# Kernel optimization log

Measured on AMD Instinct MI355X. Metric: run time of the kernel, lower is better.

Reference implementation:

```python
import jax, jax.numpy as jnp
import numpy as np
from functools import partial

EPS = 1e-12  # F.normalize eps (clamp_min on the norm)


def conv2d(x, w, b, groups=1):
    # x: [B, Cin, H, W], w: [Cout, Cin//groups, 3, 3], 'same' padding, stride 1
    y = jax.lax.conv_general_dilated(
        x, w, window_strides=(1, 1), padding='SAME',
        dimension_numbers=('NCHW', 'OIHW', 'NCHW'),
        feature_group_count=groups)
    return y + b[None, :, None, None]


def setup_inputs() -> dict:
    key = jax.random.key(0)
    ks = jax.random.split(key, 8)
    B, C, H, W = 16, 256, 32, 32
    HW = H * W
    T = 2  # tasks: seg, depth
    return {
        'features_seg': jax.random.normal(ks[0], (B, C, H, W), jnp.float32),
        'features_depth': jax.random.normal(ks[1], (B, C, H, W), jnp.float32),
        'proj_w_seg': jax.random.normal(ks[2], (C, C, 3, 3), jnp.float32) * 0.02,
        'proj_b_seg': jnp.zeros((C,), jnp.float32),
        'proj_w_depth': jax.random.normal(ks[3], (C, C, 3, 3), jnp.float32) * 0.02,
        'proj_b_depth': jnp.zeros((C,), jnp.float32),
        'fusion_w': jax.random.normal(ks[4], (HW, T, 3, 3), jnp.float32) * 0.02,
        'fusion_b': jnp.zeros((HW,), jnp.float32),
    }


def reference(features_seg, features_depth, proj_w_seg, proj_b_seg,
              proj_w_depth, proj_b_depth, fusion_w, fusion_b):
    gamma = 0.5
    feats = [features_seg, features_depth]
    proj = [(proj_w_seg, proj_b_seg), (proj_w_depth, proj_b_depth)]
    B, C, H, W = features_seg.shape
    HW = H * W

    # Per-task cosine-similarity affinity matrices [B, HW, HW]
    Ms = []
    for f in feats:
        fv = f.reshape(B, C, HW)
        fn = fv / jnp.maximum(jnp.linalg.norm(fv, axis=1, keepdims=True), EPS)
        aff = jnp.einsum('bci,bcj->bij', fn, fn)  # [B, HW, HW]
        Ms.append(aff.reshape(B, HW, H, W))

    # Stack on dim=2 then flatten -> interleaved channels [B, HW*T, H, W]
    M = jnp.stack(Ms, axis=2).reshape(B, -1, H, W)
    M = conv2d(M, fusion_w, fusion_b, groups=HW)  # [B, HW, H, W]

    attention = M.reshape(B, HW, HW).transpose(0, 2, 1)  # [B, HW, HW]

    outs = []
    for f, (w, b) in zip(feats, proj):
        value = conv2d(f, w, b).reshape(B, C, HW)          # [B, C, HW]
        attended = jnp.einsum('bck,bkj->bcj', value, attention)
        attended = attended.reshape(B, C, H, W)
        outs.append(gamma * attended + (1.0 - gamma) * f)
    return tuple(outs)
```

## Files before the change

### kernel.cpp

```cpp
#include <hip/hip_runtime.h>
#include <hip/hip_bf16.h>

typedef __bf16 bf16;
typedef __attribute__((ext_vector_type(8))) __bf16 bf16x8;
typedef __attribute__((ext_vector_type(4))) __bf16 bf16x4v;
typedef __attribute__((ext_vector_type(4))) float f32x4;

#define B_  16
#define C_  256
#define HW_ 1024

__device__ __forceinline__ void gll16(const bf16* g, bf16* l) {
  __builtin_amdgcn_global_load_lds((const __attribute__((address_space(1))) void*)g,
                                   (__attribute__((address_space(3))) void*)l, 16, 0, 0);
}

__global__ void prep_kernel(const float* __restrict__ f0, const float* __restrict__ f1,
                            bf16* __restrict__ fT, float* __restrict__ rn) {
  __shared__ float sm[256][33];
  __shared__ float ps[8][32];
  int z = blockIdx.y, t = z >> 4, b = z & 15;
  int k0 = blockIdx.x * 32;
  int tid = threadIdx.x;
  const float* fb = (t ? f1 : f0) + (size_t)b * C_ * HW_ + k0;
  int kk = tid & 31, cg = tid >> 5;
  float ssq = 0.f;
  #pragma unroll
  for (int i = 0; i < 32; ++i) {
    int c = cg + i * 8;
    float v = fb[(size_t)c * HW_ + kk];
    sm[c][kk] = v;
    ssq += v * v;
  }
  ps[cg][kk] = ssq;
  __syncthreads();
  if (tid < 32) {
    float s = 0.f;
    #pragma unroll
    for (int r = 0; r < 8; ++r) s += ps[r][tid];
    rn[z * 1024 + k0 + tid] = 1.f / fmaxf(sqrtf(s), 1e-12f);
  }
  int kl = tid >> 3, c0 = (tid & 7) * 32;
  bf16* dst = fT + ((size_t)z * HW_ + k0 + kl) * C_ + c0;
  #pragma unroll
  for (int u = 0; u < 4; ++u) {
    bf16x8 vv;
    #pragma unroll
    for (int e = 0; e < 8; ++e) vv[e] = (bf16)sm[c0 + u * 8 + e][kl];
    *(bf16x8*)(dst + u * 8) = vv;
  }
}

__global__ void fusion_conv2(const bf16* __restrict__ aff, const float* __restrict__ fw,
                             const float* __restrict__ fb, bf16* __restrict__ M) {
  __shared__ float sa[2][1024];
  int bi = blockIdx.x;
  int i = bi & 1023, b = bi >> 10;
  int tid = threadIdx.x;
  #pragma unroll
  for (int t = 0; t < 2; ++t) {
    const bf16* arow = aff + (((size_t)t * 16 + b) * 1024 + i) * 1024;
    bf16x4v ch = ((const bf16x4v*)arow)[tid];
    sa[t][tid * 4 + 0] = (float)ch[0];
    sa[t][tid * 4 + 1] = (float)ch[1];
    sa[t][tid * 4 + 2] = (float)ch[2];
    sa[t][tid * 4 + 3] = (float)ch[3];
  }
  float wgt[2][9];
  #pragma unroll
  for (int t = 0; t < 2; ++t)
    #pragma unroll
    for (int q = 0; q < 9; ++q) wgt[t][q] = fw[i * 18 + t * 9 + q];
  float bias = fb[i];
  __syncthreads();
  #pragma unroll
  for (int s0 = 0; s0 < 4; ++s0) {
    int s = tid + s0 * 256;
    int h = s >> 5, w = s & 31;
    float acc = bias;
    #pragma unroll
    for (int kh = 0; kh < 3; ++kh) {
      int hh = h + kh - 1;
      if ((unsigned)hh < 32u) {
        #pragma unroll
        for (int kw = 0; kw < 3; ++kw) {
          int ww = w + kw - 1;
          if ((unsigned)ww < 32u) {
            acc += wgt[0][kh * 3 + kw] * sa[0][hh * 32 + ww];
            acc += wgt[1][kh * 3 + kw] * sa[1][hh * 32 + ww];
          }
        }
      }
    }
    M[((size_t)bi << 10) + s] = (bf16)acc;
  }
}

__global__ void reorder_w(const float* __restrict__ w0, const float* __restrict__ w1,
                          bf16* __restrict__ y) {
  int i = blockIdx.x * 256 + threadIdx.x;
  int t = i / 589824, r2 = i % 589824;
  int c = r2 / 2304, r = r2 % 2304;
  int cin = r / 9, d = r % 9;
  y[(size_t)t * 589824 + c * 2304 + d * 256 + cin] = (bf16)(t ? w1 : w0)[r2];
}

template<int MODE, int TN>
__global__ __launch_bounds__(256)
void gemm_nt(const bf16* __restrict__ A, long long sA,
             const bf16* __restrict__ Bm, long long sB, int K,
             bf16* __restrict__ Cb, long long sC,
             const float* __restrict__ x0, const float* __restrict__ x1,
             float* __restrict__ Co) {
  constexpr int FJ   = (TN == 128) ? 4 : 2;
  __shared__ bf16 As[128 * 64];
  __shared__ bf16 Bs[TN * ((MODE == 3) ? 72 : 64)];
  const int z = blockIdx.z, t = z >> 4;
  const bf16* Ab = A + (size_t)(MODE == 3 ? t : z) * sA;
  const bf16* Bb = Bm + (size_t)(MODE == 2 ? (z & 15) : z) * sB;
  const int m0 = blockIdx.y * 128, n0 = blockIdx.x * TN;
  const int tid = threadIdx.x;
  const int lane = tid & 63, wave = tid >> 6;
  const int wm = (wave >> 1) * 64, wn = (wave & 1) * (TN / 2);
  const int fr = lane & 15, fq = lane >> 4;

  f32x4 acc[4][FJ];
  #pragma unroll
  for (int i = 0; i < 4; ++i)
    #pragma unroll
    for (int j = 0; j < FJ; ++j) acc[i][j] = 0.f;

  for (int k0 = 0; k0 < K; k0 += 64) {
    #pragma unroll
    for (int s = 0; s < 4; ++s) {
      int q = (wave * 4 + s) * 64 + lane;
      int row = q >> 3, c = (q & 7) ^ (row & 7);
      int lb = __builtin_amdgcn_readfirstlane((wave * 4 + s) * 512);
      gll16(Ab + (size_t)(m0 + row) * K + k0 + c * 8, As + lb);
    }
    if (MODE == 3) {
      int d = k0 >> 8;
      int kh = d / 3 - 1, kw = d % 3 - 1;
      int cin0 = k0 & 255;
      #pragma unroll
      for (int s = 0; s < TN / 32; ++s) {
        int q = tid + s * 256;
        int row = q >> 3, col = (q & 7) * 8;
        int j = n0 + row;
        int h = (j >> 5) + kh, w = (j & 31) + kw;
        float4 v = make_float4(0.f, 0.f, 0.f, 0.f);
        if ((unsigned)h < 32u && (unsigned)w < 32u)
          v = *(const float4*)(Bb + (size_t)(h * 32 + w) * C_ + cin0 + col);
        *(float4*)(&Bs[row * 72 + col]) = v;
      }
    } else {
      #pragma unroll
      for (int s = 0; s < TN / 32; ++s) {
        int q = (wave * (TN / 32) + s) * 64 + lane;
        int row = q >> 3, c = (q & 7) ^ (row & 7);
        int lb = __builtin_amdgcn_readfirstlane((wave * (TN / 32) + s) * 512);
        gll16(Bb + (size_t)(n0 + row) * K + k0 + c * 8, Bs + lb);
      }
    }
    __syncthreads();
    #pragma unroll
    for (int kk = 0; kk < 64; kk += 32) {
      bf16x8 af[4], bfr[FJ];
      #pragma unroll
      for (int i = 0; i < 4; ++i) {
        int rr = wm + i * 16 + fr;
        int p = ((kk >> 3) + fq) ^ (rr & 7);
        af[i] = *(const bf16x8*)(&As[rr * 64 + p * 8]);
      }
      #pragma unroll
      for (int j = 0; j < FJ; ++j) {
        int rr = wn + j * 16 + fr;
        if (MODE == 3) {
          bfr[j] = *(const bf16x8*)(&Bs[rr * 72 + kk + fq * 8]);
        } else {
          int p = ((kk >> 3) + fq) ^ (rr & 7);
          bfr[j] = *(const bf16x8*)(&Bs[rr * 64 + p * 8]);
        }
      }
      #pragma unroll
      for (int i = 0; i < 4; ++i)
        #pragma unroll
        for (int j = 0; j < FJ; ++j)
          acc[i][j] = __builtin_amdgcn_mfma_f32_16x16x32_bf16(af[i], bfr[j], acc[i][j], 0, 0, 0);
    }
    __syncthreads();
  }

  #pragma unroll
  for (int i = 0; i < 4; ++i) {
    int rbase = m0 + wm + i * 16 + fq * 4;
    #pragma unroll
    for (int j = 0; j < FJ; ++j) {
      int col = n0 + wn + j * 16 + fr;
      float cj = (MODE == 1) ? x0[(size_t)z * 1024 + col] : 0.f;
      #pragma unroll
      for (int r = 0; r < 4; ++r) {
        int row = rbase + r;
        float v = acc[i][j][r];
        if (MODE == 1) {
          Cb[(size_t)z * sC + (size_t)row * 1024 + col] =
              (bf16)(v * x0[(size_t)z * 1024 + row] * cj);
        } else if (MODE == 3) {
          const float* bias = t ? x1 : x0;
          Cb[(size_t)z * sC + (size_t)row * 1024 + col] = (bf16)(v + bias[row]);
        } else {
          const float* fp = t ? x1 : x0;
          Co[(size_t)z * sC + (size_t)row * 1024 + col] =
              0.5f * v + 0.5f * fp[(size_t)(z & 15) * sC + (size_t)row * 1024 + col];
        }
      }
    }
  }
}

extern "C" void kernel_launch(void* const* d_in, const int* in_sizes, int n_in,
                              void* d_out, int out_size, void* d_ws, size_t ws_size,
                              hipStream_t stream) {
  const float* f0 = (const float*)d_in[0];
  const float* f1 = (const float*)d_in[1];
  const float* w0 = (const float*)d_in[2];
  const float* b0 = (const float*)d_in[3];
  const float* w1 = (const float*)d_in[4];
  const float* b1 = (const float*)d_in[5];
  const float* fusion_w = (const float*)d_in[6];
  const float* fusion_b = (const float*)d_in[7];
  float* out = (float*)d_out;

  char* ws = (char*)d_ws;
  bf16* Mbuf  = (bf16*)ws;
  bf16* aff   = (bf16*)(ws + 33554432ull);
  bf16* Wr    = (bf16*)(ws + 33554432ull);
  bf16* value = (bf16*)(ws + 35913728ull);
  bf16* fT    = (bf16*)(ws + 100663296ull);
  float* rn   = (float*)(ws + 117440512ull);

  prep_kernel<<<dim3(32, 32), 256, 0, stream>>>(f0, f1, fT, rn);
  gemm_nt<1, 128><<<dim3(8, 8, 32), 256, 0, stream>>>(
      fT, (long long)HW_ * C_, fT, (long long)HW_ * C_, C_,
      aff, (long long)HW_ * HW_, rn, rn, nullptr);
  fusion_conv2<<<16384, 256, 0, stream>>>(aff, fusion_w, fusion_b, Mbuf);
  reorder_w<<<4608, 256, 0, stream>>>(w0, w1, Wr);
  gemm_nt<3, 64><<<dim3(16, 2, 32), 256, 0, stream>>>(
      Wr, 589824LL, fT, (long long)HW_ * C_, 2304,
      value, (long long)C_ * HW_, b0, b1, nullptr);
  gemm_nt<2, 64><<<dim3(16, 2, 32), 256, 0, stream>>>(
      value, (long long)C_ * HW_, Mbuf, (long long)HW_ * HW_, 1024,
      nullptr, (long long)C_ * HW_, f0, f1, out);
}
```

Baseline: 266.1 us.

## Zero-pad transposed features so conv GEMM uses async direct-to-LDS loads

The transposed bf16 feature buffer is now written into a zero-padded 34x34 spatial grid, cleared each call with a memset. The implicit-conv GEMM can then fetch its B tiles with unguarded global_load_lds into the swizzled LDS layout, instead of bounds-checked register loads into a padded LDS tile. The affinity GEMM addresses the same padded layout. The affinity and fusion output buffers are also aliased in the workspace. The trade-off is an extra memset of about 19 MB and more complex address arithmetic.

```diff
diff --git a/kernel.cpp b/kernel.cpp
--- a/kernel.cpp
+++ b/kernel.cpp
@@ -9,6 +9,8 @@
 #define B_  16
 #define C_  256
 #define HW_ 1024
+#define PADR 1156
+#define ZSTR 295936
 
 __device__ __forceinline__ void gll16(const bf16* g, bf16* l) {
   __builtin_amdgcn_global_load_lds((const __attribute__((address_space(1))) void*)g,
@@ -16,7 +18,7 @@
 }
 
 __global__ void prep_kernel(const float* __restrict__ f0, const float* __restrict__ f1,
-                            bf16* __restrict__ fT, float* __restrict__ rn) {
+                            bf16* __restrict__ fTpad, float* __restrict__ rn) {
   __shared__ float sm[256][33];
   __shared__ float ps[8][32];
   int z = blockIdx.y, t = z >> 4, b = z & 15;
@@ -40,13 +42,13 @@
     for (int r = 0; r < 8; ++r) s += ps[r][tid];
     rn[z * 1024 + k0 + tid] = 1.f / fmaxf(sqrtf(s), 1e-12f);
   }
-  int kl = tid >> 3, c0 = (tid & 7) * 32;
-  bf16* dst = fT + ((size_t)z * HW_ + k0 + kl) * C_ + c0;
+  int wl = tid >> 3, c0 = (tid & 7) * 32;
+  bf16* dst = fTpad + ((size_t)z * PADR + (blockIdx.x + 1) * 34 + wl + 1) * C_ + c0;
   #pragma unroll
   for (int u = 0; u < 4; ++u) {
     bf16x8 vv;
     #pragma unroll
-    for (int e = 0; e < 8; ++e) vv[e] = (bf16)sm[c0 + u * 8 + e][kl];
+    for (int e = 0; e < 8; ++e) vv[e] = (bf16)sm[c0 + u * 8 + e][wl];
     *(bf16x8*)(dst + u * 8) = vv;
   }
 }
@@ -112,9 +114,9 @@
              bf16* __restrict__ Cb, long long sC,
              const float* __restrict__ x0, const float* __restrict__ x1,
              float* __restrict__ Co) {
-  constexpr int FJ   = (TN == 128) ? 4 : 2;
+  constexpr int FJ = (TN == 128) ? 4 : 2;
   __shared__ bf16 As[128 * 64];
-  __shared__ bf16 Bs[TN * ((MODE == 3) ? 72 : 64)];
+  __shared__ bf16 Bs[TN * 64];
   const int z = blockIdx.z, t = z >> 4;
   const bf16* Ab = A + (size_t)(MODE == 3 ? t : z) * sA;
   const bf16* Bb = Bm + (size_t)(MODE == 2 ? (z & 15) : z) * sB;
@@ -136,30 +138,38 @@
       int q = (wave * 4 + s) * 64 + lane;
       int row = q >> 3, c = (q & 7) ^ (row & 7);
       int lb = __builtin_amdgcn_readfirstlane((wave * 4 + s) * 512);
-      gll16(Ab + (size_t)(m0 + row) * K + k0 + c * 8, As + lb);
-    }
-    if (MODE == 3) {
-      int d = k0 >> 8;
-      int kh = d / 3 - 1, kw = d % 3 - 1;
-      int cin0 = k0 & 255;
-      #pragma unroll
-      for (int s = 0; s < TN / 32; ++s) {
-        int q = tid + s * 256;
-        int row = q >> 3, col = (q & 7) * 8;
-        int j = n0 + row;
-        int h = (j >> 5) + kh, w = (j & 31) + kw;
-        float4 v = make_float4(0.f, 0.f, 0.f, 0.f);
-        if ((unsigned)h < 32u && (unsigned)w < 32u)
-          v = *(const float4*)(Bb + (size_t)(h * 32 + w) * C_ + cin0 + col);
-        *(float4*)(&Bs[row * 72 + col]) = v;
-      }
-    } else {
+      const bf16* src;
+      if (MODE == 1) {
+        int j = m0 + row;
+        src = Ab + (size_t)(((j >> 5) + 1) * 34 + (j & 31) + 1) * C_ + k0 + c * 8;
+      } else {
+        src = Ab + (size_t)(m0 + row) * K + k0 + c * 8;
+      }
+      gll16(src, As + lb);
+    }
+    {
+      int kh = 0, kw = 0, cin0 = 0;
+      if (MODE == 3) {
+        int d = k0 >> 8;
+        kh = d / 3 - 1; kw = d % 3 - 1; cin0 = k0 & 255;
+      }
       #pragma unroll
       for (int s = 0; s < TN / 32; ++s) {
         int q = (wave * (TN / 32) + s) * 64 + lane;
         int row = q >> 3, c = (q & 7) ^ (row & 7);
         int lb = __builtin_amdgcn_readfirstlane((wave * (TN / 32) + s) * 512);
-        gll16(Bb + (size_t)(n0 + row) * K + k0 + c * 8, Bs + lb);
+        const bf16* src;
+        if (MODE == 3) {
+          int j = n0 + row;
+          int h = (j >> 5) + kh, w = (j & 31) + kw;
+          src = Bb + (size_t)((h + 1) * 34 + (w + 1)) * C_ + cin0 + c * 8;
+        } else if (MODE == 1) {
+          int j = n0 + row;
+          src = Bb + (size_t)(((j >> 5) + 1) * 34 + (j & 31) + 1) * C_ + k0 + c * 8;
+        } else {
+          src = Bb + (size_t)(n0 + row) * K + k0 + c * 8;
+        }
+        gll16(src, Bs + lb);
       }
     }
     __syncthreads();
@@ -175,12 +185,8 @@
       #pragma unroll
       for (int j = 0; j < FJ; ++j) {
         int rr = wn + j * 16 + fr;
-        if (MODE == 3) {
-          bfr[j] = *(const bf16x8*)(&Bs[rr * 72 + kk + fq * 8]);
-        } else {
-          int p = ((kk >> 3) + fq) ^ (rr & 7);
-          bfr[j] = *(const bf16x8*)(&Bs[rr * 64 + p * 8]);
-        }
+        int p = ((kk >> 3) + fq) ^ (rr & 7);
+        bfr[j] = *(const bf16x8*)(&Bs[rr * 64 + p * 8]);
       }
       #pragma unroll
       for (int i = 0; i < 4; ++i)
@@ -232,21 +238,22 @@
   float* out = (float*)d_out;
 
   char* ws = (char*)d_ws;
+  bf16* aff   = (bf16*)ws;
   bf16* Mbuf  = (bf16*)ws;
-  bf16* aff   = (bf16*)(ws + 33554432ull);
   bf16* Wr    = (bf16*)(ws + 33554432ull);
   bf16* value = (bf16*)(ws + 35913728ull);
-  bf16* fT    = (bf16*)(ws + 100663296ull);
-  float* rn   = (float*)(ws + 117440512ull);
-
-  prep_kernel<<<dim3(32, 32), 256, 0, stream>>>(f0, f1, fT, rn);
+  bf16* fTpad = (bf16*)(ws + 67108864ull);
+  float* rn   = (float*)(ws + 86048768ull);
+
+  hipMemsetAsync(fTpad, 0, 18939904ull, stream);
+  prep_kernel<<<dim3(32, 32), 256, 0, stream>>>(f0, f1, fTpad, rn);
   gemm_nt<1, 128><<<dim3(8, 8, 32), 256, 0, stream>>>(
-      fT, (long long)HW_ * C_, fT, (long long)HW_ * C_, C_,
+      fTpad, ZSTR, fTpad, ZSTR, C_,
       aff, (long long)HW_ * HW_, rn, rn, nullptr);
   fusion_conv2<<<16384, 256, 0, stream>>>(aff, fusion_w, fusion_b, Mbuf);
   reorder_w<<<4608, 256, 0, stream>>>(w0, w1, Wr);
   gemm_nt<3, 64><<<dim3(16, 2, 32), 256, 0, stream>>>(
-      Wr, 589824LL, fT, (long long)HW_ * C_, 2304,
+      Wr, 589824LL, fTpad, ZSTR, 2304,
       value, (long long)C_ * HW_, b0, b1, nullptr);
   gemm_nt<2, 64><<<dim3(16, 2, 32), 256, 0, stream>>>(
       value, (long long)C_ * HW_, Mbuf, (long long)HW_ * HW_, 1024,
```

Result: no change. 263.6 us (-1.0%).
